# Performance work log

Measured on AMD Instinct MI355X. Metric: run time of the kernel, lower is better.

Reference implementation:

```python
import jax, jax.numpy as jnp
import numpy as np

# static config matching init_kwargs / input_specs
D = 768      # dim
H = 12       # num_heads
HD = D // H  # head_dim = 64
C = 38       # in_chans (AlternatingAttention default)
B = 4
T = 256
N = C * T    # 9728
SCALE = HD ** -0.5
EPS = 1e-5   # LayerNorm eps
HID = 4 * D  # mlp hidden


def setup_inputs() -> dict:
    key = jax.random.key(0)
    ks = jax.random.split(key, 6)
    w = lambda k, sh: (jax.random.normal(k, sh, jnp.float32) * 0.02)
    return {
        "x": jax.random.normal(ks[0], (B, N, D), jnp.float32),
        "norm1_w": jnp.ones((D,), jnp.float32),
        "norm1_b": jnp.zeros((D,), jnp.float32),
        "qkv_w": w(ks[1], (3 * D, D)),            # nn.Linear(dim, 3*dim, bias=False)
        "proj_w": w(ks[2], (D, D)),
        "proj_b": jnp.zeros((D,), jnp.float32),
        "norm2_w": jnp.ones((D,), jnp.float32),
        "norm2_b": jnp.zeros((D,), jnp.float32),
        "fc1_w": w(ks[3], (HID, D)),
        "fc1_b": jnp.zeros((HID,), jnp.float32),
        "fc2_w": w(ks[4], (D, HID)),
        "fc2_b": jnp.zeros((D,), jnp.float32),
    }


def _ln(x, w, b):
    m = x.mean(-1, keepdims=True)
    v = ((x - m) ** 2).mean(-1, keepdims=True)
    return (x - m) * jax.lax.rsqrt(v + EPS) * w + b


def _attn(x, qkv_w, proj_w, proj_b):
    # x: (Bc, Nn, D) -- manual (non-fused) SDPA as in the torch module
    Bc, Nn, _ = x.shape
    qkv = (x @ qkv_w.T).reshape(Bc, Nn, 3, H, HD)
    q, k, v = jnp.moveaxis(qkv, 2, 0)             # each (Bc, Nn, H, HD)
    q = jnp.swapaxes(q, 1, 2) * SCALE             # (Bc, H, Nn, HD)
    k = jnp.swapaxes(k, 1, 2)
    v = jnp.swapaxes(v, 1, 2)
    attn = jax.nn.softmax(q @ jnp.swapaxes(k, -2, -1), axis=-1)  # (Bc,H,Nn,Nn)
    o = attn @ v                                  # (Bc, H, Nn, HD)
    o = jnp.swapaxes(o, 1, 2).reshape(Bc, Nn, D)
    return o @ proj_w.T + proj_b


def reference(x, norm1_w, norm1_b, qkv_w, proj_w, proj_b,
              norm2_w, norm2_b, fc1_w, fc1_b, fc2_w, fc2_b):
    # Attention branch: block_idx=1 -> time-axis attention
    h = _ln(x, norm1_w, norm1_b)
    h = h.reshape(B, C, T, D).reshape(B * C, T, D)   # 'B (C T) D -> (B C) T D'
    h = _attn(h, qkv_w, proj_w, proj_b)
    h = h.reshape(B, C, T, D).reshape(B, N, D)       # '(B C) T D -> B (C T) D'
    x = x + h                                        # ls1 = Identity, drop_path = Identity
    # MLP branch
    h2 = _ln(x, norm2_w, norm2_b)
    h2 = jax.nn.gelu(h2 @ fc1_w.T + fc1_b, approximate=False)
    h2 = h2 @ fc2_w.T + fc2_b
    return x + h2
```

## Files before the change

kernel.cpp:

```cpp
#include <hip/hip_runtime.h>
#include <stdint.h>

#define DD 768
#define HH 12
#define HDIM 64
#define TT 256
#define BCN 152
#define MROWS 38912
#define HID 3072

typedef __attribute__((ext_vector_type(8))) short bf16x8;
typedef __attribute__((ext_vector_type(4))) float f32x4;

__device__ __forceinline__ float b2f(unsigned short u) {
  union { unsigned int i; float f; } c; c.i = ((unsigned int)u) << 16; return c.f;
}
__device__ __forceinline__ unsigned short f2b(float f) {
  union { float f; unsigned int i; } c; c.f = f;
  unsigned int x = c.i;
  return (unsigned short)((x + 0x7fffu + ((x >> 16) & 1u)) >> 16);
}

__device__ __forceinline__ void gload16(const unsigned short* g, unsigned short* l) {
  __builtin_amdgcn_global_load_lds(
      (const __attribute__((address_space(1))) void*)g,
      (__attribute__((address_space(3))) void*)l, 16, 0, 0);
}

__global__ __launch_bounds__(256) void k_cvt(const float* __restrict__ in,
                                             unsigned short* __restrict__ out, int n4) {
  int i = blockIdx.x * 256 + threadIdx.x;
  if (i >= n4) return;
  float4 a = ((const float4*)in)[i];
  ushort4 u;
  u.x = f2b(a.x); u.y = f2b(a.y); u.z = f2b(a.z); u.w = f2b(a.w);
  ((ushort4*)out)[i] = u;
}

__global__ __launch_bounds__(256) void k_ln(const float* __restrict__ x,
                                            const float* __restrict__ w,
                                            const float* __restrict__ b,
                                            unsigned short* __restrict__ out) {
  int lane = threadIdx.x & 63;
  int wv = threadIdx.x >> 6;
  size_t row = (size_t)blockIdx.x * 4 + wv;
  const float4* xr = (const float4*)(x + row * DD);
  float4 v0 = xr[lane], v1 = xr[lane + 64], v2 = xr[lane + 128];
  float s = v0.x + v0.y + v0.z + v0.w + v1.x + v1.y + v1.z + v1.w + v2.x + v2.y + v2.z + v2.w;
  float q = v0.x*v0.x + v0.y*v0.y + v0.z*v0.z + v0.w*v0.w
          + v1.x*v1.x + v1.y*v1.y + v1.z*v1.z + v1.w*v1.w
          + v2.x*v2.x + v2.y*v2.y + v2.z*v2.z + v2.w*v2.w;
#pragma unroll
  for (int m = 1; m < 64; m <<= 1) { s += __shfl_xor(s, m, 64); q += __shfl_xor(q, m, 64); }
  float mean = s * (1.0f / 768.0f);
  float var = q * (1.0f / 768.0f) - mean * mean;
  float rstd = rsqrtf(var + 1e-5f);
  ushort4* orow = (ushort4*)(out + row * DD);
#pragma unroll
  for (int i = 0; i < 3; i++) {
    int idx = lane + i * 64;
    float4 v = (i == 0) ? v0 : (i == 1) ? v1 : v2;
    float4 ww = ((const float4*)w)[idx];
    float4 bb = ((const float4*)b)[idx];
    ushort4 u;
    u.x = f2b((v.x - mean) * rstd * ww.x + bb.x);
    u.y = f2b((v.y - mean) * rstd * ww.y + bb.y);
    u.z = f2b((v.z - mean) * rstd * ww.z + bb.z);
    u.w = f2b((v.w - mean) * rstd * ww.w + bb.w);
    orow[idx] = u;
  }
}


template <int MH>
__device__ __forceinline__ void read_a(const unsigned short* Al, bf16x8 (&af)[4][2],
                                       int wr, int cl, int hi) {
#pragma unroll
  for (int mi = 0; mi < 4; mi++)
#pragma unroll
    for (int ks = 0; ks < 2; ks++) {
      int row = MH * 128 + wr * 64 + mi * 16 + cl;
      af[mi][ks] = *(const bf16x8*)&Al[row * 64 + (((ks * 4 + hi) ^ (row & 7)) * 8)];
    }
}

template <int G>
__device__ __forceinline__ void read_b(const unsigned short* Bl, bf16x8 (&bfr)[2][2][2],
                                       int wc, int cl, int hi) {
#pragma unroll
  for (int ni = 0; ni < 2; ni++)
#pragma unroll
    for (int ks = 0; ks < 2; ks++) {
      int row = G * 128 + wc * 32 + ni * 16 + cl;
      bfr[G][ni][ks] = *(const bf16x8*)&Bl[row * 64 + (((ks * 4 + hi) ^ (row & 7)) * 8)];
    }
}

template <int MH, int G>
__device__ __forceinline__ void mfma_q(f32x4 (&acc)[2][4][2][2], const bf16x8 (&af)[4][2],
                                       const bf16x8 (&bfr)[2][2][2]) {
  __builtin_amdgcn_s_setprio(1);
#pragma unroll
  for (int mi = 0; mi < 4; mi++)
#pragma unroll
    for (int ni = 0; ni < 2; ni++)
#pragma unroll
      for (int ks = 0; ks < 2; ks++)
        acc[MH][mi][G][ni] = __builtin_amdgcn_mfma_f32_16x16x32_bf16(
            af[mi][ks], bfr[G][ni][ks], acc[MH][mi][G][ni], 0, 0, 0);
  __builtin_amdgcn_s_setprio(0);
}

#define VM4   asm volatile("s_waitcnt vmcnt(4)" ::: "memory")
#define LGKM0 do { asm volatile("s_waitcnt lgkmcnt(0)" ::: "memory"); \
                   __builtin_amdgcn_sched_barrier(0); } while (0)
#define BAR   __builtin_amdgcn_s_barrier()

template <int MODE>
__global__ __launch_bounds__(512, 2) void k_gemm3(const unsigned short* __restrict__ A,
                                                  const unsigned short* __restrict__ W,
                                                  const float* __restrict__ bias,
                                                  const float* resid,
                                                  void* outv, int N, int K) {
  __shared__ __align__(16) unsigned short As[2][256 * 64];
  __shared__ __align__(16) unsigned short Bs[2][256 * 64];
  const int tid = threadIdx.x;
  const int lane = tid & 63, wv = tid >> 6;
  const int wr = wv >> 2, wc = wv & 3;
  const int cl = lane & 15, hi = lane >> 4;

  const int nbx = gridDim.x;
  const int nwg = nbx * gridDim.y;
  const int flat = blockIdx.y * nbx + blockIdx.x;
  const int swz = (flat & 7) * (nwg >> 3) + (flat >> 3);
  const int m_blk = swz / nbx, n_blk = swz % nbx;
  const size_t bm = (size_t)m_blk * 256, bn = (size_t)n_blk * 256;
  const unsigned short* Ab = A + bm * K;
  const unsigned short* Wb = W + bn * K;

  auto stA = [&](int kt, int b, int h) {
#pragma unroll
    for (int j = 0; j < 2; j++) {
      int idx = j * 512 + tid;
      int row = h * 128 + (idx >> 3);
      int cg = (idx & 7) ^ (row & 7);
      gload16(Ab + (size_t)row * K + (size_t)kt * 64 + cg * 8,
              &As[b][row * 64 + (idx & 7) * 8]);
    }
  };
  auto stB = [&](int kt, int b, int h) {
#pragma unroll
    for (int j = 0; j < 2; j++) {
      int idx = j * 512 + tid;
      int row = h * 128 + (idx >> 3);
      int cg = (idx & 7) ^ (row & 7);
      gload16(Wb + (size_t)row * K + (size_t)kt * 64 + cg * 8,
              &Bs[b][row * 64 + (idx & 7) * 8]);
    }
  };

  f32x4 acc[2][4][2][2];
#pragma unroll
  for (int a0 = 0; a0 < 2; a0++)
#pragma unroll
    for (int a1 = 0; a1 < 4; a1++)
#pragma unroll
      for (int a2 = 0; a2 < 2; a2++)
#pragma unroll
        for (int a3 = 0; a3 < 2; a3++) acc[a0][a1][a2][a3] = (f32x4){0.f, 0.f, 0.f, 0.f};

  bf16x8 af[4][2], bfr[2][2][2];
  const int nt = K >> 6;

  stA(0, 0, 0); stB(0, 0, 0); stB(0, 0, 1); stA(0, 0, 1);

  for (int t = 0; t < nt; t += 2) {
    const bool p2 = (t + 2) < nt;
    VM4; BAR;
    read_a<0>(As[0], af, wr, cl, hi);
    read_b<0>(Bs[0], bfr, wc, cl, hi);
    stA(t + 1, 1, 0);
    LGKM0;
    mfma_q<0, 0>(acc, af, bfr);
    VM4; BAR;
    read_b<1>(Bs[0], bfr, wc, cl, hi);
    stB(t + 1, 1, 0);
    LGKM0;
    mfma_q<0, 1>(acc, af, bfr);
    VM4; BAR;
    read_a<1>(As[0], af, wr, cl, hi);
    stB(t + 1, 1, 1);
    LGKM0;
    mfma_q<1, 0>(acc, af, bfr);
    BAR;
    stA(t + 1, 1, 1);
    mfma_q<1, 1>(acc, af, bfr);

    VM4; BAR;
    read_a<0>(As[1], af, wr, cl, hi);
    read_b<0>(Bs[1], bfr, wc, cl, hi);
    if (p2) stA(t + 2, 0, 0);
    LGKM0;
    mfma_q<0, 0>(acc, af, bfr);
    if (p2) { VM4; } else { asm volatile("s_waitcnt vmcnt(2)" ::: "memory"); }
    BAR;
    read_b<1>(Bs[1], bfr, wc, cl, hi);
    if (p2) stB(t + 2, 0, 0);
    LGKM0;
    mfma_q<0, 1>(acc, af, bfr);
    if (p2) { VM4; } else { asm volatile("s_waitcnt vmcnt(0)" ::: "memory"); }
    BAR;
    read_a<1>(As[1], af, wr, cl, hi);
    if (p2) stB(t + 2, 0, 1);
    LGKM0;
    mfma_q<1, 0>(acc, af, bfr);
    BAR;
    if (p2) stA(t + 2, 0, 1);
    mfma_q<1, 1>(acc, af, bfr);
  }

#pragma unroll
  for (int mh = 0; mh < 2; mh++)
#pragma unroll
    for (int mi = 0; mi < 4; mi++)
#pragma unroll
      for (int g = 0; g < 2; g++)
#pragma unroll
        for (int ni = 0; ni < 2; ni++) {
          size_t col = bn + g * 128 + wc * 32 + ni * 16 + cl;
#pragma unroll
          for (int r = 0; r < 4; r++) {
            size_t row = bm + mh * 128 + wr * 64 + mi * 16 + hi * 4 + r;
            float v = acc[mh][mi][g][ni][r];
            if (MODE == 0) {
              ((unsigned short*)outv)[row * N + col] = f2b(v);
            } else if (MODE == 1) {
              v += bias[col] + resid[row * N + col];
              ((float*)outv)[row * N + col] = v;
            } else {
              v += bias[col];
              float gg = 0.5f * v * (1.0f + erff(v * 0.70710678118654752f));
              ((unsigned short*)outv)[row * N + col] = f2b(gg);
            }
          }
        }
}

__global__ __launch_bounds__(256) void k_attn(const unsigned short* __restrict__ qkv,
                                              unsigned short* __restrict__ o) {
  __shared__ unsigned short Kc[64 * 64];
  __shared__ unsigned short Vt[64 * 64];
  __shared__ unsigned short Pl[4][64 * 64];
  int h = blockIdx.x;
  int bc = blockIdx.y;
  int tid = threadIdx.x;
  int lane = tid & 63, wv = tid >> 6;
  int cl = lane & 15, hi = lane >> 4;

  bf16x8 qf[4][2];
#pragma unroll
  for (int m = 0; m < 4; m++)
#pragma unroll
    for (int ks = 0; ks < 2; ks++) {
      size_t row = (size_t)bc * 256 + wv * 64 + m * 16 + cl;
      bf16x8 raw = *(const bf16x8*)(qkv + row * 2304 + h * 64 + ks * 32 + hi * 8);
      bf16x8 sc;
#pragma unroll
      for (int j = 0; j < 8; j++) sc[j] = (short)f2b(0.125f * b2f((unsigned short)raw[j]));
      qf[m][ks] = sc;
    }

  f32x4 oacc[4][4];
#pragma unroll
  for (int m = 0; m < 4; m++)
#pragma unroll
    for (int n = 0; n < 4; n++) oacc[m][n] = (f32x4){0.f, 0.f, 0.f, 0.f};
  float mrun[4][4], lrun[4][4];
#pragma unroll
  for (int m = 0; m < 4; m++)
#pragma unroll
    for (int r = 0; r < 4; r++) { mrun[m][r] = -1e30f; lrun[m][r] = 0.f; }

  for (int j = 0; j < 4; j++) {
    __syncthreads();
#pragma unroll
    for (int it = 0; it < 2; ++it) {
      int idx = it * 256 + tid;
      int tok = idx >> 3;
      int c8 = idx & 7;
      size_t gtok = (size_t)bc * 256 + j * 64 + tok;
      uint4 kvv = *(const uint4*)(qkv + gtok * 2304 + 768 + h * 64 + c8 * 8);
      *(uint4*)&Kc[tok * 64 + c8 * 8] = kvv;
      union { uint4 u4; unsigned short us[8]; } cv;
      cv.u4 = *(const uint4*)(qkv + gtok * 2304 + 1536 + h * 64 + c8 * 8);
#pragma unroll
      for (int jj = 0; jj < 8; jj++) Vt[(c8 * 8 + jj) * 64 + tok] = cv.us[jj];
    }
    __syncthreads();

    f32x4 s[4][4];
#pragma unroll
    for (int m = 0; m < 4; m++)
#pragma unroll
      for (int n = 0; n < 4; n++) s[m][n] = (f32x4){0.f, 0.f, 0.f, 0.f};
#pragma unroll
    for (int ks = 0; ks < 2; ++ks) {
      int ko = ks * 32 + hi * 8;
      bf16x8 kf[4];
#pragma unroll
      for (int n = 0; n < 4; n++) kf[n] = *(const bf16x8*)&Kc[(n * 16 + cl) * 64 + ko];
#pragma unroll
      for (int m = 0; m < 4; m++)
#pragma unroll
        for (int n = 0; n < 4; n++)
          s[m][n] = __builtin_amdgcn_mfma_f32_16x16x32_bf16(qf[m][ks], kf[n], s[m][n], 0, 0, 0);
    }

#pragma unroll
    for (int m = 0; m < 4; m++) {
#pragma unroll
      for (int r = 0; r < 4; r++) {
        float pm = fmaxf(fmaxf(s[m][0][r], s[m][1][r]), fmaxf(s[m][2][r], s[m][3][r]));
#pragma unroll
        for (int xm = 1; xm < 16; xm <<= 1) pm = fmaxf(pm, __shfl_xor(pm, xm, 64));
        float nm = fmaxf(mrun[m][r], pm);
        float fac = __expf(mrun[m][r] - nm);
        mrun[m][r] = nm;
        float ps = 0.f;
#pragma unroll
        for (int n = 0; n < 4; n++) {
          float e = __expf(s[m][n][r] - nm);
          s[m][n][r] = e;
          ps += e;
        }
#pragma unroll
        for (int xm = 1; xm < 16; xm <<= 1) ps += __shfl_xor(ps, xm, 64);
        lrun[m][r] = lrun[m][r] * fac + ps;
#pragma unroll
        for (int n2 = 0; n2 < 4; n2++) oacc[m][n2][r] *= fac;
      }
#pragma unroll
      for (int n = 0; n < 4; n++)
#pragma unroll
        for (int r = 0; r < 4; r++)
          Pl[wv][(m * 16 + hi * 4 + r) * 64 + n * 16 + cl] = f2b(s[m][n][r]);
    }
    __syncthreads();

#pragma unroll
    for (int ks = 0; ks < 2; ++ks) {
      int ko = ks * 32 + hi * 8;
      bf16x8 pa[4], pv[4];
#pragma unroll
      for (int m = 0; m < 4; m++) pa[m] = *(const bf16x8*)&Pl[wv][(m * 16 + cl) * 64 + ko];
#pragma unroll
      for (int n = 0; n < 4; n++) pv[n] = *(const bf16x8*)&Vt[(n * 16 + cl) * 64 + ko];
#pragma unroll
      for (int m = 0; m < 4; m++)
#pragma unroll
        for (int n = 0; n < 4; n++)
          oacc[m][n] = __builtin_amdgcn_mfma_f32_16x16x32_bf16(pa[m], pv[n], oacc[m][n], 0, 0, 0);
    }
  }

#pragma unroll
  for (int m = 0; m < 4; m++)
#pragma unroll
    for (int r = 0; r < 4; r++) {
      float inv = 1.0f / lrun[m][r];
      size_t row = (size_t)bc * 256 + wv * 64 + m * 16 + hi * 4 + r;
#pragma unroll
      for (int n = 0; n < 4; n++)
        o[row * DD + h * 64 + n * 16 + cl] = f2b(oacc[m][n][r] * inv);
    }
}

extern "C" void kernel_launch(void* const* d_in, const int* in_sizes, int n_in,
                              void* d_out, int out_size, void* d_ws, size_t ws_size,
                              hipStream_t stream) {
  const float* x     = (const float*)d_in[0];
  const float* n1w   = (const float*)d_in[1];
  const float* n1b   = (const float*)d_in[2];
  const float* qkvw  = (const float*)d_in[3];
  const float* projw = (const float*)d_in[4];
  const float* projb = (const float*)d_in[5];
  const float* n2w   = (const float*)d_in[6];
  const float* n2b   = (const float*)d_in[7];
  const float* fc1w  = (const float*)d_in[8];
  const float* fc1b  = (const float*)d_in[9];
  const float* fc2w  = (const float*)d_in[10];
  const float* fc2b  = (const float*)d_in[11];
  float* out = (float*)d_out;

  const size_t NEED = 312999936ull;
  if (ws_size < NEED) return;
  char* ws = (char*)d_ws;
  unsigned short* h   = (unsigned short*)(ws);
  unsigned short* qkv = (unsigned short*)(ws + 59768832ull);
  unsigned short* ob  = (unsigned short*)(ws + 239075328ull);
  unsigned short* act = (unsigned short*)(ws + 59768832ull);
  unsigned short* wq  = (unsigned short*)(ws + 298844160ull);
  unsigned short* wp  = wq + 2304 * 768;
  unsigned short* w1  = wp + 768 * 768;
  unsigned short* w2  = w1 + 3072 * 768;

  k_cvt<<<1728, 256, 0, stream>>>(qkvw, wq, 2304 * 768 / 4);
  k_cvt<<<576, 256, 0, stream>>>(projw, wp, 768 * 768 / 4);
  k_cvt<<<2304, 256, 0, stream>>>(fc1w, w1, 3072 * 768 / 4);
  k_cvt<<<2304, 256, 0, stream>>>(fc2w, w2, 768 * 3072 / 4);

  k_ln<<<MROWS / 4, 256, 0, stream>>>(x, n1w, n1b, h);
  k_gemm3<0><<<dim3(2304 / 256, MROWS / 256), 512, 0, stream>>>(h, wq, nullptr, nullptr, qkv, 2304, 768);
  k_attn<<<dim3(HH, BCN), 256, 0, stream>>>(qkv, ob);
  k_gemm3<1><<<dim3(768 / 256, MROWS / 256), 512, 0, stream>>>(ob, wp, projb, x, out, 768, 768);
  k_ln<<<MROWS / 4, 256, 0, stream>>>(out, n2w, n2b, h);
  k_gemm3<2><<<dim3(3072 / 256, MROWS / 256), 512, 0, stream>>>(h, w1, fc1b, nullptr, act, 3072, 768);
  k_gemm3<1><<<dim3(768 / 256, MROWS / 256), 512, 0, stream>>>(act, w2, fc2b, out, out, 768, 3072);
}
```

Baseline: 1.229 ms.

## Convert GEMMs to persistent 256-block kernel with cross-tile prefetch

Replaces the grid-per-tile GEMM launch with a persistent kernel of 256 workgroups. Each workgroup takes a contiguous range of output tiles, ordered M-major within each N column so consecutive tiles share the weight block. The last k-step of one tile prefetches the first k-slice of the next, so the load pipeline does not drain between tiles. Launch bounds drop to one workgroup per CU. This targets tail-wave imbalance and per-tile pipeline ramp-up, but gives up the latency hiding that two resident workgroups per CU provided.

```diff
diff --git a/kernel.cpp b/kernel.cpp
--- a/kernel.cpp
+++ b/kernel.cpp
@@ -8,6 +8,7 @@
 #define BCN 152
 #define MROWS 38912
 #define HID 3072
+#define MB_CNT 152
 
 typedef __attribute__((ext_vector_type(8))) short bf16x8;
 typedef __attribute__((ext_vector_type(4))) float f32x4;
@@ -117,11 +118,11 @@
 #define BAR   __builtin_amdgcn_s_barrier()
 
 template <int MODE>
-__global__ __launch_bounds__(512, 2) void k_gemm3(const unsigned short* __restrict__ A,
+__global__ __launch_bounds__(512, 1) void k_gemm4(const unsigned short* __restrict__ A,
                                                   const unsigned short* __restrict__ W,
                                                   const float* __restrict__ bias,
                                                   const float* resid,
-                                                  void* outv, int N, int K) {
+                                                  void* outv, int N, int K, int NB) {
   __shared__ __align__(16) unsigned short As[2][256 * 64];
   __shared__ __align__(16) unsigned short Bs[2][256 * 64];
   const int tid = threadIdx.x;
@@ -129,121 +130,138 @@
   const int wr = wv >> 2, wc = wv & 3;
   const int cl = lane & 15, hi = lane >> 4;
 
-  const int nbx = gridDim.x;
-  const int nwg = nbx * gridDim.y;
-  const int flat = blockIdx.y * nbx + blockIdx.x;
-  const int swz = (flat & 7) * (nwg >> 3) + (flat >> 3);
-  const int m_blk = swz / nbx, n_blk = swz % nbx;
-  const size_t bm = (size_t)m_blk * 256, bn = (size_t)n_blk * 256;
-  const unsigned short* Ab = A + bm * K;
-  const unsigned short* Wb = W + bn * K;
-
-  auto stA = [&](int kt, int b, int h) {
+  const int b = blockIdx.x;
+  const int bp = (b & 7) * 32 + (b >> 3);
+  const int ntiles = MB_CNT * NB;
+  const int q = ntiles >> 8, r = ntiles & 255;
+  const int t0 = bp < r ? bp * (q + 1) : r * (q + 1) + (bp - r) * q;
+  const int cnt = bp < r ? q + 1 : q;
+
+  auto stA = [&](const unsigned short* base, int kt, int bb, int h) {
 #pragma unroll
     for (int j = 0; j < 2; j++) {
       int idx = j * 512 + tid;
       int row = h * 128 + (idx >> 3);
       int cg = (idx & 7) ^ (row & 7);
-      gload16(Ab + (size_t)row * K + (size_t)kt * 64 + cg * 8,
-              &As[b][row * 64 + (idx & 7) * 8]);
+      gload16(base + (size_t)row * K + (size_t)kt * 64 + cg * 8,
+              &As[bb][row * 64 + (idx & 7) * 8]);
     }
   };
-  auto stB = [&](int kt, int b, int h) {
+  auto stB = [&](const unsigned short* base, int kt, int bb, int h) {
 #pragma unroll
     for (int j = 0; j < 2; j++) {
       int idx = j * 512 + tid;
       int row = h * 128 + (idx >> 3);
       int cg = (idx & 7) ^ (row & 7);
-      gload16(Wb + (size_t)row * K + (size_t)kt * 64 + cg * 8,
-              &Bs[b][row * 64 + (idx & 7) * 8]);
+      gload16(base + (size_t)row * K + (size_t)kt * 64 + cg * 8,
+              &Bs[bb][row * 64 + (idx & 7) * 8]);
     }
   };
 
   f32x4 acc[2][4][2][2];
-#pragma unroll
-  for (int a0 = 0; a0 < 2; a0++)
-#pragma unroll
-    for (int a1 = 0; a1 < 4; a1++)
-#pragma unroll
-      for (int a2 = 0; a2 < 2; a2++)
-#pragma unroll
-        for (int a3 = 0; a3 < 2; a3++) acc[a0][a1][a2][a3] = (f32x4){0.f, 0.f, 0.f, 0.f};
-
   bf16x8 af[4][2], bfr[2][2][2];
   const int nt = K >> 6;
 
-  stA(0, 0, 0); stB(0, 0, 0); stB(0, 0, 1); stA(0, 0, 1);
-
-  for (int t = 0; t < nt; t += 2) {
-    const bool p2 = (t + 2) < nt;
-    VM4; BAR;
-    read_a<0>(As[0], af, wr, cl, hi);
-    read_b<0>(Bs[0], bfr, wc, cl, hi);
-    stA(t + 1, 1, 0);
-    LGKM0;
-    mfma_q<0, 0>(acc, af, bfr);
-    VM4; BAR;
-    read_b<1>(Bs[0], bfr, wc, cl, hi);
-    stB(t + 1, 1, 0);
-    LGKM0;
-    mfma_q<0, 1>(acc, af, bfr);
-    VM4; BAR;
-    read_a<1>(As[0], af, wr, cl, hi);
-    stB(t + 1, 1, 1);
-    LGKM0;
-    mfma_q<1, 0>(acc, af, bfr);
-    BAR;
-    stA(t + 1, 1, 1);
-    mfma_q<1, 1>(acc, af, bfr);
-
-    VM4; BAR;
-    read_a<0>(As[1], af, wr, cl, hi);
-    read_b<0>(Bs[1], bfr, wc, cl, hi);
-    if (p2) stA(t + 2, 0, 0);
-    LGKM0;
-    mfma_q<0, 0>(acc, af, bfr);
-    if (p2) { VM4; } else { asm volatile("s_waitcnt vmcnt(2)" ::: "memory"); }
-    BAR;
-    read_b<1>(Bs[1], bfr, wc, cl, hi);
-    if (p2) stB(t + 2, 0, 0);
-    LGKM0;
-    mfma_q<0, 1>(acc, af, bfr);
-    if (p2) { VM4; } else { asm volatile("s_waitcnt vmcnt(0)" ::: "memory"); }
-    BAR;
-    read_a<1>(As[1], af, wr, cl, hi);
-    if (p2) stB(t + 2, 0, 1);
-    LGKM0;
-    mfma_q<1, 0>(acc, af, bfr);
-    BAR;
-    if (p2) stA(t + 2, 0, 1);
-    mfma_q<1, 1>(acc, af, bfr);
-  }
-
-#pragma unroll
-  for (int mh = 0; mh < 2; mh++)
-#pragma unroll
-    for (int mi = 0; mi < 4; mi++)
-#pragma unroll
-      for (int g = 0; g < 2; g++)
-#pragma unroll
-        for (int ni = 0; ni < 2; ni++) {
-          size_t col = bn + g * 128 + wc * 32 + ni * 16 + cl;
-#pragma unroll
-          for (int r = 0; r < 4; r++) {
-            size_t row = bm + mh * 128 + wr * 64 + mi * 16 + hi * 4 + r;
-            float v = acc[mh][mi][g][ni][r];
-            if (MODE == 0) {
-              ((unsigned short*)outv)[row * N + col] = f2b(v);
-            } else if (MODE == 1) {
-              v += bias[col] + resid[row * N + col];
-              ((float*)outv)[row * N + col] = v;
-            } else {
-              v += bias[col];
-              float gg = 0.5f * v * (1.0f + erff(v * 0.70710678118654752f));
-              ((unsigned short*)outv)[row * N + col] = f2b(gg);
+  for (int i = 0; i < cnt; i++) {
+    const int tau = t0 + i;
+    const int m_blk = tau % MB_CNT;
+    const int n_blk = tau / MB_CNT;
+    const size_t bm = (size_t)m_blk * 256, bn = (size_t)n_blk * 256;
+    const unsigned short* Ab = A + bm * K;
+    const unsigned short* Wb = W + bn * K;
+    const bool hasNext = (i + 1 < cnt);
+    const int tau2 = hasNext ? tau + 1 : tau;
+    const unsigned short* An = A + (size_t)(tau2 % MB_CNT) * 256 * K;
+    const unsigned short* Wn = W + (size_t)(tau2 / MB_CNT) * 256 * K;
+
+#pragma unroll
+    for (int a0 = 0; a0 < 2; a0++)
+#pragma unroll
+      for (int a1 = 0; a1 < 4; a1++)
+#pragma unroll
+        for (int a2 = 0; a2 < 2; a2++)
+#pragma unroll
+          for (int a3 = 0; a3 < 2; a3++) acc[a0][a1][a2][a3] = (f32x4){0.f, 0.f, 0.f, 0.f};
+
+    if (i == 0) {
+      stA(Ab, 0, 0, 0); stB(Wb, 0, 0, 0); stB(Wb, 0, 0, 1); stA(Ab, 0, 0, 1);
+    }
+
+    for (int t = 0; t < nt; t += 2) {
+      const bool lastp = (t + 2 == nt);
+      VM4; BAR;
+      read_a<0>(As[0], af, wr, cl, hi);
+      read_b<0>(Bs[0], bfr, wc, cl, hi);
+      stA(Ab, t + 1, 1, 0);
+      LGKM0;
+      mfma_q<0, 0>(acc, af, bfr);
+      VM4; BAR;
+      read_b<1>(Bs[0], bfr, wc, cl, hi);
+      stB(Wb, t + 1, 1, 0);
+      LGKM0;
+      mfma_q<0, 1>(acc, af, bfr);
+      VM4; BAR;
+      read_a<1>(As[0], af, wr, cl, hi);
+      stB(Wb, t + 1, 1, 1);
+      LGKM0;
+      mfma_q<1, 0>(acc, af, bfr);
+      BAR;
+      stA(Ab, t + 1, 1, 1);
+      mfma_q<1, 1>(acc, af, bfr);
+
+      const bool st2 = !lastp || hasNext;
+      const unsigned short* A2 = lastp ? An : Ab;
+      const unsigned short* W2 = lastp ? Wn : Wb;
+      const int k2 = lastp ? 0 : t + 2;
+      VM4; BAR;
+      read_a<0>(As[1], af, wr, cl, hi);
+      read_b<0>(Bs[1], bfr, wc, cl, hi);
+      if (st2) stA(A2, k2, 0, 0);
+      LGKM0;
+      mfma_q<0, 0>(acc, af, bfr);
+      if (st2) { VM4; } else { asm volatile("s_waitcnt vmcnt(2)" ::: "memory"); }
+      BAR;
+      read_b<1>(Bs[1], bfr, wc, cl, hi);
+      if (st2) stB(W2, k2, 0, 0);
+      LGKM0;
+      mfma_q<0, 1>(acc, af, bfr);
+      if (st2) { VM4; } else { asm volatile("s_waitcnt vmcnt(0)" ::: "memory"); }
+      BAR;
+      read_a<1>(As[1], af, wr, cl, hi);
+      if (st2) stB(W2, k2, 0, 1);
+      LGKM0;
+      mfma_q<1, 0>(acc, af, bfr);
+      BAR;
+      if (st2) stA(A2, k2, 0, 1);
+      mfma_q<1, 1>(acc, af, bfr);
+    }
+
+#pragma unroll
+    for (int mh = 0; mh < 2; mh++)
+#pragma unroll
+      for (int mi = 0; mi < 4; mi++)
+#pragma unroll
+        for (int g = 0; g < 2; g++)
+#pragma unroll
+          for (int ni = 0; ni < 2; ni++) {
+            size_t col = bn + g * 128 + wc * 32 + ni * 16 + cl;
+#pragma unroll
+            for (int rr = 0; rr < 4; rr++) {
+              size_t row = bm + mh * 128 + wr * 64 + mi * 16 + hi * 4 + rr;
+              float v = acc[mh][mi][g][ni][rr];
+              if (MODE == 0) {
+                ((unsigned short*)outv)[row * N + col] = f2b(v);
+              } else if (MODE == 1) {
+                v += bias[col] + resid[row * N + col];
+                ((float*)outv)[row * N + col] = v;
+              } else {
+                v += bias[col];
+                float gg = 0.5f * v * (1.0f + erff(v * 0.70710678118654752f));
+                ((unsigned short*)outv)[row * N + col] = f2b(gg);
+              }
             }
           }
-        }
+  }
 }
 
 __global__ __launch_bounds__(256) void k_attn(const unsigned short* __restrict__ qkv,
@@ -410,10 +428,10 @@
   k_cvt<<<2304, 256, 0, stream>>>(fc2w, w2, 768 * 3072 / 4);
 
   k_ln<<<MROWS / 4, 256, 0, stream>>>(x, n1w, n1b, h);
-  k_gemm3<0><<<dim3(2304 / 256, MROWS / 256), 512, 0, stream>>>(h, wq, nullptr, nullptr, qkv, 2304, 768);
+  k_gemm4<0><<<256, 512, 0, stream>>>(h, wq, nullptr, nullptr, qkv, 2304, 768, 9);
   k_attn<<<dim3(HH, BCN), 256, 0, stream>>>(qkv, ob);
-  k_gemm3<1><<<dim3(768 / 256, MROWS / 256), 512, 0, stream>>>(ob, wp, projb, x, out, 768, 768);
+  k_gemm4<1><<<256, 512, 0, stream>>>(ob, wp, projb, x, out, 768, 768, 3);
   k_ln<<<MROWS / 4, 256, 0, stream>>>(out, n2w, n2b, h);
-  k_gemm3<2><<<dim3(3072 / 256, MROWS / 256), 512, 0, stream>>>(h, w1, fc1b, nullptr, act, 3072, 768);
-  k_gemm3<1><<<dim3(768 / 256, MROWS / 256), 512, 0, stream>>>(act, w2, fc2b, out, out, 768, 3072);
-}
+  k_gemm4<2><<<256, 512, 0, stream>>>(h, w1, fc1b, nullptr, act, 3072, 768, 12);
+  k_gemm4<1><<<256, 512, 0, stream>>>(act, w2, fc2b, out, out, 768, 3072, 3);
+}
```

Result: no change. 1.221 ms (-0.7%).
